# Kernel tuning notes

Hardware: AMD Instinct MI355X
Metric: run time of the kernel (lower is better)

The kernel has to match this reference:

```python
import jax, jax.numpy as jnp
import numpy as np

N = 100000   # nodes per node type (A and B)
E = 500000   # edges per relation
H = 8        # n_heads
D = 32       # hidden_dim (= encoder_hidden_dim = input_dim)
IN = 32      # input feature dim
SLOPE = 0.2  # leaky relu negative slope
# relations in order: ab1 (A->B), ba1 (B->A), ab2 (A->B), ba2 (B->A)
RELS = [(0, 1), (1, 0), (0, 1), (1, 0)]  # (src_type, dst_type)
REV = [1, 0, 3, 2]                        # reverse-relation index


def _leaky(x):
    return jnp.where(x >= 0, x, SLOPE * x)


def _rel_conv(h_src, h_dst, W_src, W_dst, remb, Wr, s_idx, d_idx):
    """RelationGraphConv: GAT-style edge attention on one relation graph."""
    fs = (h_src @ W_src).reshape(-1, H, D)          # [N, H, D]
    fd = (h_dst @ W_dst).reshape(-1, H, D)          # [N, H, D]
    ra = (remb @ Wr).reshape(H, 2 * D)              # [H, 2D]
    e_dst = (fd * ra[:, :D]).sum(-1)                # [N, H]
    e_src = (fs * ra[:, D:]).sum(-1)                # [N, H]
    e = _leaky(e_src[s_idx] + e_dst[d_idx])         # [E, H]
    # edge softmax per destination node (per head)
    m = jax.ops.segment_max(e, d_idx, num_segments=N)
    m = jnp.where(jnp.isfinite(m), m, 0.0)
    ex = jnp.exp(e - m[d_idx])
    z = jax.ops.segment_sum(ex, d_idx, num_segments=N)
    a = ex / z[d_idx]                               # [E, H]
    msg = fs[s_idx] * a[:, :, None]                 # [E, H, D]
    out = jax.ops.segment_sum(msg, d_idx, num_segments=N)  # [N, H, D]
    return jax.nn.relu(out.reshape(N, H * D))


def _crossing(stacked, w):
    """RelationCrossing over relations targeting one dst type.
    stacked: [R, N, H*D], w: [H, D]"""
    f = stacked.reshape(stacked.shape[0], N, H, D)
    att = (f * w).sum(-1, keepdims=True)            # [R, N, H, 1]
    att = jax.nn.softmax(_leaky(att), axis=0)
    return (f * att).sum(0).reshape(N, H * D)


def setup_inputs() -> dict:
    key = jax.random.key(0)
    ks = jax.random.split(key, 12)
    xn = lambda k, shape, s=1.0: jax.random.normal(k, shape, jnp.float32) * s
    return {
        "feat":    xn(ks[0], (4, N, IN)),
        "rel_emb": xn(ks[1], (4, IN)),
        "W_node":  xn(ks[2], (2, IN, H * D), 0.1),
        "W_rel":   xn(ks[3], (4, IN, H * 2 * D), 0.1),
        "W_prop":  xn(ks[4], (4, IN, H * D), 0.1),
        "b_prop":  xn(ks[5], (4, H * D), 0.1),
        "W_res":   xn(ks[6], (2, IN, H * D), 0.1),
        "b_res":   xn(ks[7], (2, H * D), 0.1),
        "alpha":   xn(ks[8], (2,)),
        "Wx":      xn(ks[9], (2, H, D), 0.1),
        "src": jax.random.randint(ks[10], (4, E), 0, N),
        "dst": jax.random.randint(ks[11], (4, E), 0, N),
    }


def reference(feat, rel_emb, W_node, W_rel, W_prop, b_prop, W_res, b_res,
              alpha, Wx, src, dst):
    outs = []
    for r in range(4):  # fixed small set of relations
        st, dt = RELS[r]
        # src feats come from the reverse relation's dst-node features
        o = _rel_conv(feat[REV[r]], feat[r], W_node[st], W_node[dt],
                      rel_emb[r], W_rel[r], src[r], dst[r])
        # residual connection (eval mode, dropout = identity)
        a = jax.nn.sigmoid(alpha[dt])
        res = feat[r] @ W_res[dt] + b_res[dt]
        outs.append(o * a + res * (1.0 - a))
    # relation crossing per dst node type
    cross_A = _crossing(jnp.stack([outs[1], outs[3]]), Wx[0])
    cross_B = _crossing(jnp.stack([outs[0], outs[2]]), Wx[1])
    node_out = jnp.stack([cross_A, cross_B])                  # [2, N, H*D]
    # relation propagation (Linear per etype)
    rel_out = jnp.einsum('ri,rio->ro', rel_emb, W_prop) + b_prop  # [4, H*D]
    return node_out, rel_out
```

## Files before the change

kernel.cpp:

```cpp
#include <hip/hip_runtime.h>
#include <hip/hip_bf16.h>

#define NN 100000
#define EE 500000
#define H 8
#define D 32
#define INF_ 32
#define HD 256
#define SLOPE 0.2f
#define L_ (4 * NN)
#define NB_ ((L_ + 255) / 256)

typedef unsigned short u16;
typedef unsigned int u32;
typedef short bf16x8 __attribute__((ext_vector_type(8)));
typedef float f32x4 __attribute__((ext_vector_type(4)));

union U8 { uint4 u; bf16x8 v; };

__device__ __forceinline__ float leaky(float x) { return x >= 0.f ? x : SLOPE * x; }
__device__ __forceinline__ u16 bf16r(float x) {
    u32 u = __float_as_uint(x);
    u += 0x7fffu + ((u >> 16) & 1u);
    return (u16)(u >> 16);
}
__device__ __forceinline__ float bf16f(u16 v) { return __uint_as_float((u32)v << 16); }
__device__ __forceinline__ u32 cvtpk(float lo, float hi) {
    u32 r;
    asm("v_cvt_pk_bf16_f32 %0, %1, %2" : "=v"(r) : "v"(lo), "v"(hi));
    return r;
}

__global__ void k_prep(const float* __restrict__ rel_emb, const float* __restrict__ W_rel,
                       const float* __restrict__ W_prop, const float* __restrict__ b_prop,
                       float* __restrict__ ra, float* __restrict__ rel_out) {
    int idx = blockIdx.x * blockDim.x + threadIdx.x;
    if (idx < 4 * 512) {
        int r = idx >> 9, o = idx & 511;
        float s = 0.f;
        #pragma unroll
        for (int i = 0; i < INF_; ++i) s += rel_emb[r * INF_ + i] * W_rel[(r * INF_ + i) * 512 + o];
        ra[idx] = s;
    } else if (idx < 4 * 512 + 4 * 256) {
        int j = idx - 2048;
        int r = j >> 8;
        float s = b_prop[j];
        #pragma unroll
        for (int i = 0; i < INF_; ++i) s += rel_emb[r * INF_ + i] * W_prop[(r * INF_ + i) * 256 + (j & 255)];
        rel_out[j] = s;
    }
}

__global__ void k_wfrag(const float* __restrict__ W_node, const float* __restrict__ W_res,
                        const float* __restrict__ ra, u16* __restrict__ Wfrag) {
    int idx = blockIdx.x * 256 + threadIdx.x;
    if (idx >= 68 * 512) return;
    int lb = idx & 511;
    int l = lb >> 3, b = lb & 7;
    int k = (l >> 4) * 8 + b, i = l & 15;
    float v;
    if (idx < 4 * 512) {
        int q = idx >> 9;
        int rq = q ^ 1;
        const float* W = W_node + (size_t)(q & 1) * 32 * 256;
        int h = i & 7;
        const float* rr = (i < 8) ? (ra + q * 512 + h * 64 + 32) : (ra + rq * 512 + h * 64);
        float s = 0.f;
        #pragma unroll
        for (int j = 0; j < 32; ++j) s += W[k * 256 + h * 32 + j] * rr[j];
        v = s;
    } else if (idx < 36 * 512) {
        int j = idx - 4 * 512;
        int ty = j >> 13;
        int ct = (j & 8191) >> 9;
        v = W_node[(size_t)ty * 32 * 256 + k * 256 + ct * 16 + i];
    } else {
        int j = idx - 36 * 512;
        int ty = j >> 13;
        int ct = (j & 8191) >> 9;
        v = W_res[(size_t)ty * 32 * 256 + k * 256 + ct * 16 + i];
    }
    Wfrag[idx] = bf16r(v);
}

__global__ __launch_bounds__(256) void k_score(const float* __restrict__ feat,
                                               const u16* __restrict__ Wfrag,
                                               char* __restrict__ pk) {
    const int q = blockIdx.y, rq = q ^ 1;
    const int t = threadIdx.x, lane = t & 63;
    const int li = lane & 15, g = lane >> 4;
    const int wid = blockIdx.x * 4 + (t >> 6);
    const int nw = gridDim.x * 4;
    f32x4 zz = {0.f, 0.f, 0.f, 0.f};
    U8 a;
    a.u = *(const uint4*)(Wfrag + ((size_t)q * 64 + lane) * 8);
    const float* F = feat + (size_t)rq * NN * INF_;
    char* pkq = pk + (size_t)q * NN * 128;
    for (int tile = wid; tile < NN / 16; tile += nw) {
        const int node = tile * 16 + li;
        const float* fp = F + node * 32 + g * 8;
        float4 f0 = *(const float4*)fp;
        float4 f1 = *(const float4*)(fp + 4);
        U8 b;
        b.u.x = cvtpk(f0.x, f0.y); b.u.y = cvtpk(f0.z, f0.w);
        b.u.z = cvtpk(f1.x, f1.y); b.u.w = cvtpk(f1.z, f1.w);
        char* rec = pkq + (size_t)node * 128;
        *(uint4*)(rec + 32 + g * 16) = b.u;
        f32x4 sc = __builtin_amdgcn_mfma_f32_16x16x32_bf16(a.v, b.v, zz, 0, 0, 0);
        char* sp = rec + ((g < 2) ? g * 16 : 96 + (g - 2) * 16);
        *(float4*)sp = make_float4(sc[0], sc[1], sc[2], sc[3]);
    }
}

__global__ void k_count(const int* __restrict__ dst, u32* __restrict__ deg, u32* __restrict__ epos) {
    int idx = blockIdx.x * blockDim.x + threadIdx.x;
    if (idx >= 4 * EE) return;
    int r = idx / EE;
    epos[idx] = atomicAdd(&deg[r * NN + dst[idx]], 1u);
}

__global__ void k_scan1(const u32* __restrict__ deg, u32* __restrict__ incl, u32* __restrict__ bsum) {
    __shared__ u32 sm[256];
    const int t = threadIdx.x;
    int i = blockIdx.x * 256 + t;
    u32 v = (i < L_) ? deg[i] : 0u;
    sm[t] = v;
    __syncthreads();
    for (int ofs = 1; ofs < 256; ofs <<= 1) {
        u32 x = (t >= ofs) ? sm[t - ofs] : 0u;
        __syncthreads();
        sm[t] += x;
        __syncthreads();
    }
    if (i < L_) incl[i] = sm[t];
    if (t == 255) bsum[blockIdx.x] = sm[255];
}

__global__ void k_scan2(const u32* __restrict__ bsum, u32* __restrict__ bofs) {
    __shared__ u32 sm[256];
    __shared__ u32 runS;
    const int t = threadIdx.x;
    if (t == 0) runS = 0u;
    __syncthreads();
    for (int c = 0; c < NB_; c += 256) {
        u32 v = (c + t < NB_) ? bsum[c + t] : 0u;
        sm[t] = v;
        __syncthreads();
        for (int ofs = 1; ofs < 256; ofs <<= 1) {
            u32 x = (t >= ofs) ? sm[t - ofs] : 0u;
            __syncthreads();
            sm[t] += x;
            __syncthreads();
        }
        u32 excl = sm[t] - v;
        if (c + t < NB_) bofs[c + t] = runS + excl;
        __syncthreads();
        if (t == 255) runS += sm[255];
        __syncthreads();
    }
}

__global__ void k_scan3(const u32* __restrict__ deg, const u32* __restrict__ incl,
                        const u32* __restrict__ bofs, u32* __restrict__ offsets) {
    int i = blockIdx.x * 256 + threadIdx.x;
    if (i >= L_) return;
    offsets[i] = incl[i] - deg[i] + bofs[i >> 8];
}

__global__ void k_fill(const int* __restrict__ src, const int* __restrict__ dst,
                       const u32* __restrict__ offsets, const u32* __restrict__ epos,
                       int* __restrict__ esorted) {
    int idx = blockIdx.x * blockDim.x + threadIdx.x;
    if (idx >= 4 * EE) return;
    int r = idx / EE;
    esorted[offsets[r * NN + dst[idx]] + epos[idx]] = src[idx];
}

template <int W>
__device__ __forceinline__ void procW(const int* __restrict__ ep,
                                      const char* __restrict__ pkr,
                                      int h, int fq, float ed,
                                      float& z, float& a0, float& a1, float& a2, float& a3) {
    int s[W];
    #pragma unroll
    for (int j = 0; j < W; ++j) s[j] = ep[j];
    float e[W];
    ushort4 f[W];
    #pragma unroll
    for (int j = 0; j < W; ++j) {
        const char* rec = pkr + (size_t)s[j] * 128;
        e[j] = *(const float*)(rec + h * 4);
        f[j] = *(const ushort4*)(rec + 32 + fq * 8);
    }
    float w[W];
    #pragma unroll
    for (int j = 0; j < W; ++j) w[j] = __expf(leaky(e[j] + ed));
    #pragma unroll
    for (int j = 0; j < W; ++j) {
        z += w[j];
        a0 = fmaf(bf16f(f[j].x), w[j], a0);
        a1 = fmaf(bf16f(f[j].y), w[j], a1);
        a2 = fmaf(bf16f(f[j].z), w[j], a2);
        a3 = fmaf(bf16f(f[j].w), w[j], a3);
    }
}

__global__ __launch_bounds__(256) void k_msg_final(const u32* __restrict__ offsets,
                                                   const u32* __restrict__ deg,
                                                   const int* __restrict__ esorted,
                                                   const char* __restrict__ pk,
                                                   const u16* __restrict__ Wfrag,
                                                   const float* __restrict__ b_res,
                                                   const float* __restrict__ alpha,
                                                   const float* __restrict__ Wx,
                                                   float* __restrict__ outp) {
    const int ty = blockIdx.y;
    const int rA = ty ? 0 : 1, rB = ty ? 2 : 3;
    const int t = threadIdx.x, lane = t & 63, w = t >> 6;
    const int tile = blockIdx.x;
    __shared__ uint4 lag[2][16][33];

    u32 odv;
    {
        int seg = lane >> 4, nl0 = lane & 15;
        int ii = ((seg < 2) ? rA : rB) * NN + tile * 16 + nl0;
        odv = (seg & 1) ? deg[ii] : offsets[ii];
    }

    {
        const int h = lane >> 3, fq = lane & 7;
        #pragma unroll 1
        for (int uu = 0; uu < 8; ++uu) {
            const int unit = uu * 4 + w;
            const int rs = unit >> 4, nl = unit & 15;
            const int r = rs ? rB : rA;
            const int node = tile * 16 + nl;
            const u32 off = __shfl(odv, (rs << 5) + nl, 64);
            const u32 dg  = __shfl(odv, (rs << 5) + 16 + nl, 64);
            uint2 st = {0u, 0u};
            if (dg) {
                const float ed = *(const float*)(pk + ((size_t)(r ^ 1) * NN + node) * 128 + 96 + h * 4);
                const char* pkr = pk + (size_t)r * NN * 128;
                const int* ep = esorted + off;
                float z = 0.f, a0 = 0.f, a1 = 0.f, a2 = 0.f, a3 = 0.f;
                u32 k = 0;
                for (; k + 8 <= dg; k += 8)
                    procW<8>(ep + k, pkr, h, fq, ed, z, a0, a1, a2, a3);
                u32 rem = dg - k;
                if (rem & 4) { procW<4>(ep + k, pkr, h, fq, ed, z, a0, a1, a2, a3); k += 4; }
                if (rem & 2) { procW<2>(ep + k, pkr, h, fq, ed, z, a0, a1, a2, a3); k += 2; }
                if (rem & 1) { procW<1>(ep + k, pkr, h, fq, ed, z, a0, a1, a2, a3); }
                float inv = 1.f / z;
                st.x = cvtpk(a0 * inv, a1 * inv);
                st.y = cvtpk(a2 * inv, a3 * inv);
            }
            *((uint2*)lag[rs][nl] + h * 8 + fq) = st;
        }
    }
    __syncthreads();

    const int li = lane & 15, g = lane >> 4;
    const int node = tile * 16 + li;
    const float ga = 1.f / (1.f + __expf(-alpha[ty]));
    const float gb = 1.f - ga;
    f32x4 zz = {0.f, 0.f, 0.f, 0.f};
    const u16* WnF = Wfrag + (size_t)(4 + (1 - ty) * 16) * 512;
    const u16* WrF = Wfrag + (size_t)(36 + ty * 16) * 512;

    U8 fA, fB;
    fA.u = *(const uint4*)(pk + ((size_t)(rA ^ 1) * NN + node) * 128 + 32 + g * 16);
    fB.u = *(const uint4*)(pk + ((size_t)(rB ^ 1) * NN + node) * 128 + 32 + g * 16);
    float* op = outp + ((size_t)ty * NN + node) * HD;

    #pragma unroll
    for (int hh = 0; hh < 2; ++hh) {
        const int h = w + hh * 4;
        U8 ag1, ag2;
        ag1.u = lag[0][li][h * 4 + g];
        ag2.u = lag[1][li][h * 4 + g];
        float o1[8], o2[8];
        float s1 = 0.f, s2 = 0.f;
        #pragma unroll
        for (int c2 = 0; c2 < 2; ++c2) {
            const int ct = h * 2 + c2;
            U8 wn, wr;
            wn.u = *(const uint4*)(WnF + ((size_t)ct * 64 + lane) * 8);
            wr.u = *(const uint4*)(WrF + ((size_t)ct * 64 + lane) * 8);
            f32x4 m1 = __builtin_amdgcn_mfma_f32_16x16x32_bf16(wn.v, ag1.v, zz, 0, 0, 0);
            f32x4 m2 = __builtin_amdgcn_mfma_f32_16x16x32_bf16(wn.v, ag2.v, zz, 0, 0, 0);
            f32x4 r1 = __builtin_amdgcn_mfma_f32_16x16x32_bf16(wr.v, fA.v, zz, 0, 0, 0);
            f32x4 r2 = __builtin_amdgcn_mfma_f32_16x16x32_bf16(wr.v, fB.v, zz, 0, 0, 0);
            float4 bv = *(const float4*)(b_res + ty * 256 + ct * 16 + g * 4);
            float4 wv = *(const float4*)(Wx + ty * 256 + ct * 16 + g * 4);
            #pragma unroll
            for (int j = 0; j < 4; ++j) {
                float bj = (&bv.x)[j], wj = (&wv.x)[j];
                float v1 = fmaxf(m1[j], 0.f) * ga + (r1[j] + bj) * gb;
                float v2 = fmaxf(m2[j], 0.f) * ga + (r2[j] + bj) * gb;
                o1[c2 * 4 + j] = v1;
                o2[c2 * 4 + j] = v2;
                s1 += v1 * wj;
                s2 += v2 * wj;
            }
        }
        s1 += __shfl_xor(s1, 16, 64);
        s1 += __shfl_xor(s1, 32, 64);
        s2 += __shfl_xor(s2, 16, 64);
        s2 += __shfl_xor(s2, 32, 64);
        float a1l = leaky(s1), a2l = leaky(s2);
        float mx = fmaxf(a1l, a2l);
        float e1 = __expf(a1l - mx), e2 = __expf(a2l - mx);
        float inv = 1.f / (e1 + e2);
        float wa = e1 * inv, wb = e2 * inv;
        #pragma unroll
        for (int c2 = 0; c2 < 2; ++c2) {
            const int ct = h * 2 + c2;
            float4 o;
            #pragma unroll
            for (int j = 0; j < 4; ++j)
                (&o.x)[j] = o1[c2 * 4 + j] * wa + o2[c2 * 4 + j] * wb;
            *(float4*)(op + ct * 16 + g * 4) = o;
        }
    }
}

extern "C" void kernel_launch(void* const* d_in, const int* in_sizes, int n_in,
                              void* d_out, int out_size, void* d_ws, size_t ws_size,
                              hipStream_t stream) {
    const float* feat    = (const float*)d_in[0];
    const float* rel_emb = (const float*)d_in[1];
    const float* W_node  = (const float*)d_in[2];
    const float* W_rel   = (const float*)d_in[3];
    const float* W_prop  = (const float*)d_in[4];
    const float* b_prop  = (const float*)d_in[5];
    const float* W_res   = (const float*)d_in[6];
    const float* b_res   = (const float*)d_in[7];
    const float* alpha   = (const float*)d_in[8];
    const float* Wx      = (const float*)d_in[9];
    const int*   src     = (const int*)d_in[10];
    const int*   dst     = (const int*)d_in[11];
    float* out = (float*)d_out;

    char* ws = (char*)d_ws;
    float* ra      = (float*)ws;
    char*  pk      = ws + 8192;
    u16*   Wfrag   = (u16*)(pk + (size_t)4 * NN * 128);
    u32*   deg     = (u32*)((char*)Wfrag + 68 * 512 * 2);
    u32*   offsets = deg + L_;
    u32*   incl    = offsets + L_;
    u32*   bsum    = incl + L_;
    u32*   bofs    = bsum + 2048;
    u32*   epos    = bofs + 2048;
    int*   esorted = (int*)(epos + (size_t)4 * EE);

    hipMemsetAsync(deg, 0, (size_t)L_ * 4, stream);

    k_prep<<<12, 256, 0, stream>>>(rel_emb, W_rel, W_prop, b_prop, ra, out + (size_t)2 * NN * HD);
    k_wfrag<<<136, 256, 0, stream>>>(W_node, W_res, ra, Wfrag);

    int eb = (4 * EE + 255) / 256;
    k_count<<<eb, 256, 0, stream>>>(dst, deg, epos);
    k_scan1<<<NB_, 256, 0, stream>>>(deg, incl, bsum);
    k_scan2<<<1, 256, 0, stream>>>(bsum, bofs);
    k_scan3<<<NB_, 256, 0, stream>>>(deg, incl, bofs, offsets);
    k_fill<<<eb, 256, 0, stream>>>(src, dst, offsets, epos, esorted);

    k_score<<<dim3(512, 4), 256, 0, stream>>>(feat, Wfrag, pk);

    k_msg_final<<<dim3(NN / 16, 2), 256, 0, stream>>>(offsets, deg, esorted, pk,
                                                      Wfrag, b_res, alpha, Wx, out);
}
```

Measured before the change: 417.7 us.

## Precompute per-edge attention weights in a separate kernel and split packed node records

```diff
diff --git a/kernel.cpp b/kernel.cpp
--- a/kernel.cpp
+++ b/kernel.cpp
@@ -85,7 +85,8 @@
 
 __global__ __launch_bounds__(256) void k_score(const float* __restrict__ feat,
                                                const u16* __restrict__ Wfrag,
-                                               char* __restrict__ pk) {
+                                               float* __restrict__ sc2,
+                                               u16* __restrict__ fb) {
     const int q = blockIdx.y, rq = q ^ 1;
     const int t = threadIdx.x, lane = t & 63;
     const int li = lane & 15, g = lane >> 4;
@@ -95,7 +96,7 @@
     U8 a;
     a.u = *(const uint4*)(Wfrag + ((size_t)q * 64 + lane) * 8);
     const float* F = feat + (size_t)rq * NN * INF_;
-    char* pkq = pk + (size_t)q * NN * 128;
+    u16* fbq = fb + (size_t)q * NN * 32;
     for (int tile = wid; tile < NN / 16; tile += nw) {
         const int node = tile * 16 + li;
         const float* fp = F + node * 32 + g * 8;
@@ -104,10 +105,10 @@
         U8 b;
         b.u.x = cvtpk(f0.x, f0.y); b.u.y = cvtpk(f0.z, f0.w);
         b.u.z = cvtpk(f1.x, f1.y); b.u.w = cvtpk(f1.z, f1.w);
-        char* rec = pkq + (size_t)node * 128;
-        *(uint4*)(rec + 32 + g * 16) = b.u;
+        *(uint4*)(fbq + node * 32 + g * 8) = b.u;
         f32x4 sc = __builtin_amdgcn_mfma_f32_16x16x32_bf16(a.v, b.v, zz, 0, 0, 0);
-        char* sp = rec + ((g < 2) ? g * 16 : 96 + (g - 2) * 16);
+        float* sp = (g < 2) ? (sc2 + ((size_t)q * NN + node) * 16 + (g & 1) * 4)
+                            : (sc2 + ((size_t)rq * NN + node) * 16 + 8 + (g - 2) * 4);
         *(float4*)sp = make_float4(sc[0], sc[1], sc[2], sc[3]);
     }
 }
@@ -169,32 +170,41 @@
 
 __global__ void k_fill(const int* __restrict__ src, const int* __restrict__ dst,
                        const u32* __restrict__ offsets, const u32* __restrict__ epos,
-                       int* __restrict__ esorted) {
+                       int2* __restrict__ esorted2) {
     int idx = blockIdx.x * blockDim.x + threadIdx.x;
     if (idx >= 4 * EE) return;
     int r = idx / EE;
-    esorted[offsets[r * NN + dst[idx]] + epos[idx]] = src[idx];
+    int d = dst[idx];
+    esorted2[offsets[r * NN + d] + epos[idx]] = make_int2(src[idx], d);
+}
+
+__global__ void k_escore(const int2* __restrict__ es2, const float* __restrict__ sc2,
+                         float* __restrict__ w8) {
+    int gid = blockIdx.x * 256 + threadIdx.x;
+    if (gid >= 4 * EE * 8) return;
+    int p = gid >> 3, h = gid & 7;
+    int r = p / EE;
+    int2 sd = es2[p];
+    float es = sc2[((size_t)r * NN + sd.x) * 16 + h];
+    float ed = sc2[((size_t)r * NN + sd.y) * 16 + 8 + h];
+    w8[(size_t)p * 8 + h] = __expf(leaky(es + ed));
 }
 
 template <int W>
-__device__ __forceinline__ void procW(const int* __restrict__ ep,
-                                      const char* __restrict__ pkr,
-                                      int h, int fq, float ed,
+__device__ __forceinline__ void procW(const int2* __restrict__ ep,
+                                      const float* __restrict__ wp,
+                                      const u16* __restrict__ fbr,
+                                      int h, int fq,
                                       float& z, float& a0, float& a1, float& a2, float& a3) {
     int s[W];
     #pragma unroll
-    for (int j = 0; j < W; ++j) s[j] = ep[j];
-    float e[W];
+    for (int j = 0; j < W; ++j) s[j] = ep[j].x;
+    float w[W];
+    #pragma unroll
+    for (int j = 0; j < W; ++j) w[j] = wp[j * 8 + h];
     ushort4 f[W];
     #pragma unroll
-    for (int j = 0; j < W; ++j) {
-        const char* rec = pkr + (size_t)s[j] * 128;
-        e[j] = *(const float*)(rec + h * 4);
-        f[j] = *(const ushort4*)(rec + 32 + fq * 8);
-    }
-    float w[W];
-    #pragma unroll
-    for (int j = 0; j < W; ++j) w[j] = __expf(leaky(e[j] + ed));
+    for (int j = 0; j < W; ++j) f[j] = *(const ushort4*)(fbr + (size_t)s[j] * 32 + fq * 4);
     #pragma unroll
     for (int j = 0; j < W; ++j) {
         z += w[j];
@@ -207,8 +217,9 @@
 
 __global__ __launch_bounds__(256) void k_msg_final(const u32* __restrict__ offsets,
                                                    const u32* __restrict__ deg,
-                                                   const int* __restrict__ esorted,
-                                                   const char* __restrict__ pk,
+                                                   const int2* __restrict__ esorted2,
+                                                   const float* __restrict__ w8,
+                                                   const u16* __restrict__ fb,
                                                    const u16* __restrict__ Wfrag,
                                                    const float* __restrict__ b_res,
                                                    const float* __restrict__ alpha,
@@ -234,22 +245,21 @@
             const int unit = uu * 4 + w;
             const int rs = unit >> 4, nl = unit & 15;
             const int r = rs ? rB : rA;
-            const int node = tile * 16 + nl;
             const u32 off = __shfl(odv, (rs << 5) + nl, 64);
             const u32 dg  = __shfl(odv, (rs << 5) + 16 + nl, 64);
             uint2 st = {0u, 0u};
             if (dg) {
-                const float ed = *(const float*)(pk + ((size_t)(r ^ 1) * NN + node) * 128 + 96 + h * 4);
-                const char* pkr = pk + (size_t)r * NN * 128;
-                const int* ep = esorted + off;
+                const u16* fbr = fb + (size_t)r * NN * 32;
+                const int2* ep = esorted2 + off;
+                const float* wp = w8 + (size_t)off * 8;
                 float z = 0.f, a0 = 0.f, a1 = 0.f, a2 = 0.f, a3 = 0.f;
                 u32 k = 0;
                 for (; k + 8 <= dg; k += 8)
-                    procW<8>(ep + k, pkr, h, fq, ed, z, a0, a1, a2, a3);
+                    procW<8>(ep + k, wp + (size_t)k * 8, fbr, h, fq, z, a0, a1, a2, a3);
                 u32 rem = dg - k;
-                if (rem & 4) { procW<4>(ep + k, pkr, h, fq, ed, z, a0, a1, a2, a3); k += 4; }
-                if (rem & 2) { procW<2>(ep + k, pkr, h, fq, ed, z, a0, a1, a2, a3); k += 2; }
-                if (rem & 1) { procW<1>(ep + k, pkr, h, fq, ed, z, a0, a1, a2, a3); }
+                if (rem & 4) { procW<4>(ep + k, wp + (size_t)k * 8, fbr, h, fq, z, a0, a1, a2, a3); k += 4; }
+                if (rem & 2) { procW<2>(ep + k, wp + (size_t)k * 8, fbr, h, fq, z, a0, a1, a2, a3); k += 2; }
+                if (rem & 1) { procW<1>(ep + k, wp + (size_t)k * 8, fbr, h, fq, z, a0, a1, a2, a3); }
                 float inv = 1.f / z;
                 st.x = cvtpk(a0 * inv, a1 * inv);
                 st.y = cvtpk(a2 * inv, a3 * inv);
@@ -268,8 +278,8 @@
     const u16* WrF = Wfrag + (size_t)(36 + ty * 16) * 512;
 
     U8 fA, fB;
-    fA.u = *(const uint4*)(pk + ((size_t)(rA ^ 1) * NN + node) * 128 + 32 + g * 16);
-    fB.u = *(const uint4*)(pk + ((size_t)(rB ^ 1) * NN + node) * 128 + 32 + g * 16);
+    fA.u = *(const uint4*)(fb + ((size_t)(rA ^ 1) * NN + node) * 32 + g * 8);
+    fB.u = *(const uint4*)(fb + ((size_t)(rB ^ 1) * NN + node) * 32 + g * 8);
     float* op = outp + ((size_t)ty * NN + node) * HD;
 
     #pragma unroll
@@ -343,15 +353,17 @@
 
     char* ws = (char*)d_ws;
     float* ra      = (float*)ws;
-    char*  pk      = ws + 8192;
-    u16*   Wfrag   = (u16*)(pk + (size_t)4 * NN * 128);
+    u16*   fb      = (u16*)(ws + 8192);
+    float* sc2     = (float*)((char*)fb + (size_t)4 * NN * 64);
+    u16*   Wfrag   = (u16*)((char*)sc2 + (size_t)4 * NN * 64);
     u32*   deg     = (u32*)((char*)Wfrag + 68 * 512 * 2);
     u32*   offsets = deg + L_;
     u32*   incl    = offsets + L_;
     u32*   bsum    = incl + L_;
     u32*   bofs    = bsum + 2048;
     u32*   epos    = bofs + 2048;
-    int*   esorted = (int*)(epos + (size_t)4 * EE);
+    int2*  esorted2 = (int2*)(epos + (size_t)4 * EE);
+    float* w8      = (float*)(esorted2 + (size_t)4 * EE);
 
     hipMemsetAsync(deg, 0, (size_t)L_ * 4, stream);
 
@@ -363,10 +375,11 @@
     k_scan1<<<NB_, 256, 0, stream>>>(deg, incl, bsum);
     k_scan2<<<1, 256, 0, stream>>>(bsum, bofs);
     k_scan3<<<NB_, 256, 0, stream>>>(deg, incl, bofs, offsets);
-    k_fill<<<eb, 256, 0, stream>>>(src, dst, offsets, epos, esorted);
-
-    k_score<<<dim3(512, 4), 256, 0, stream>>>(feat, Wfrag, pk);
-
-    k_msg_final<<<dim3(NN / 16, 2), 256, 0, stream>>>(offsets, deg, esorted, pk,
+    k_fill<<<eb, 256, 0, stream>>>(src, dst, offsets, epos, esorted2);
+
+    k_score<<<dim3(512, 4), 256, 0, stream>>>(feat, Wfrag, sc2, fb);
+    k_escore<<<62500, 256, 0, stream>>>(esorted2, sc2, w8);
+
+    k_msg_final<<<dim3(NN / 16, 2), 256, 0, stream>>>(offsets, deg, esorted2, w8, fb,
                                                       Wfrag, b_res, alpha, Wx, out);
 }
```

Measured after the change: 440.3 us. +5.4%, slower.
